# Performance work log

Measured on AMD Instinct MI355X. Metric: run time of the kernel, lower is better.

## Reference

```python
import jax, jax.numpy as jnp
import numpy as np

VOCAB_SIZE = 4096
D_EMBED = 256
BETA = 0.25  # unused: module returns raw commit_loss; beta applied by caller


def setup_inputs() -> dict:
    key = jax.random.key(0)
    k_h, k_e = jax.random.split(key)
    h = jax.random.normal(k_h, (16, D_EMBED, 32, 32), dtype=jnp.float32)
    embedding = jax.random.normal(k_e, (VOCAB_SIZE, D_EMBED), dtype=jnp.float32)
    return {"h": h, "embedding": embedding}


def reference(h, embedding):
    B, C, H, W = h.shape
    h = h.astype(jnp.float32)
    # (B, C, H, W) -> (N, C) with N = B*H*W
    h_flat = jnp.transpose(h, (0, 2, 3, 1)).reshape(-1, C)
    dist = (
        jnp.sum(h_flat * h_flat, axis=1, keepdims=True)
        + jnp.sum(embedding * embedding, axis=1)
        - 2.0 * jnp.einsum("nc,vc->nv", h_flat, embedding)
    )
    indices_flat = jnp.argmin(dist, axis=1)
    indices = indices_flat.reshape(B, H, W)
    # gather codebook vectors and restore (B, C, H, W)
    z_q = jnp.transpose(embedding[indices_flat].reshape(B, H, W, C), (0, 3, 1, 2))
    commit_loss = jnp.mean((h - jax.lax.stop_gradient(z_q)) ** 2)
    # straight-through estimator
    z_q_st = h + jax.lax.stop_gradient(z_q - h)
    return z_q_st, indices, commit_loss
```

## Files before the change

kernel.cpp:

```cpp
#include <hip/hip_runtime.h>

#define D 256
#define VOCAB 4096
#define NTOT 16384
#define N_OUT0 4194304

typedef _Float16 half8 __attribute__((ext_vector_type(8)));
typedef float f32x4 __attribute__((ext_vector_type(4)));

__device__ __forceinline__ void gld16(const void* g, void* l) {
    __builtin_amdgcn_global_load_lds(
        (const __attribute__((address_space(1))) void*)g,
        (__attribute__((address_space(3))) void*)l, 16, 0, 0);
}

__device__ __forceinline__ unsigned long long pack_key(float d, int v) {
    unsigned u = __float_as_uint(d);
    u ^= ((unsigned)((int)u >> 31)) | 0x80000000u;
    return ((unsigned long long)u << 32) | (unsigned)v;
}

__global__ __launch_bounds__(64) void k_prep(const float* __restrict__ emb,
                                             float* __restrict__ esq,
                                             unsigned long long* __restrict__ gbest,
                                             float* __restrict__ out2) {
    const int v = blockIdx.x, lane = threadIdx.x;
    float4 e = *(const float4*)(emb + (size_t)v * D + lane * 4);
    float s = e.x * e.x + e.y * e.y + e.z * e.z + e.w * e.w;
#pragma unroll
    for (int m = 32; m >= 1; m >>= 1) s += __shfl_xor(s, m, 64);
    if (lane == 0) esq[v] = s;
    if (v < NTOT / 64) gbest[(size_t)v * 64 + lane] = ~0ULL;
    if (v == 0 && lane == 0) out2[0] = 0.0f;
}

__global__ __launch_bounds__(256) void k_pack(const float* __restrict__ h,
                                              const float* __restrict__ emb,
                                              _Float16* __restrict__ Apk,
                                              _Float16* __restrict__ Bpk) {
    __shared__ float S[8192];
    const int tid = threadIdx.x;
    const int bid = blockIdx.x;
    if (bid < 512) {
        const int bm = bid >> 3, w = bid & 7;
        const int b = bm >> 2, p0 = (bm & 3) * 256;
        const float* src = h + ((size_t)b << 18) + p0;
#pragma unroll 4
        for (int cl = 0; cl < 32; ++cl)
            S[cl * 256 + tid] = src[(size_t)(w * 32 + cl) << 10 | (unsigned)tid];
        __syncthreads();
        _Float16* dstT = Apk + (size_t)bm * 131072 + (size_t)w * 16384;
#pragma unroll
        for (int i = 0; i < 4; ++i) {
            alignas(16) _Float16 hi[8], lo[8];
#pragma unroll
            for (int j = 0; j < 8; ++j) {
                float vv = S[(i * 8 + j) * 256 + tid];
                _Float16 hv = (_Float16)vv;
                hi[j] = hv;
                lo[j] = (_Float16)(vv - (float)hv);
            }
            _Float16* dst = dstT + i * 2048 + tid * 8;
            *(half8*)dst = *(half8*)hi;
            *(half8*)(dst + 8192) = *(half8*)lo;
        }
    } else {
        const int bid2 = bid - 512;
        const int bn = bid2 >> 3, w = bid2 & 7;
        const int v0 = bn * 128;
#pragma unroll 4
        for (int i = 0; i < 16; ++i) {
            int flat = i * 256 + tid;
            int r = flat >> 5, cl = flat & 31;
            S[cl * 129 + r] = emb[(size_t)(v0 + r) * D + w * 32 + cl];
        }
        __syncthreads();
        _Float16* dstT = Bpk + (size_t)bn * 65536 + (size_t)w * 8192;
#pragma unroll
        for (int i = 0; i < 2; ++i) {
            int s = i * 256 + tid;
            int q = s >> 7, r = s & 127;
            alignas(16) _Float16 hi[8], lo[8];
#pragma unroll
            for (int j = 0; j < 8; ++j) {
                float vv = S[(q * 8 + j) * 129 + r];
                _Float16 hv = (_Float16)vv;
                hi[j] = hv;
                lo[j] = (_Float16)(vv - (float)hv);
            }
            _Float16* dst = dstT + q * 1024 + r * 8;
            *(half8*)dst = *(half8*)hi;
            *(half8*)(dst + 4096) = *(half8*)lo;
        }
    }
}


#define STAGE_A_HI(W, NB) do { const _Float16* s_ = Ag + (W) * 16384; \
    gld16(s_ + tid * 8, As + (NB) + tid * 8); \
    gld16(s_ + 4096 + tid * 8, As + (NB) + 4096 + tid * 8); } while (0)
#define STAGE_A_LO(W, NB) do { const _Float16* s_ = Ag + (W) * 16384 + 8192; \
    gld16(s_ + tid * 8, As + (NB) + 8192 + tid * 8); \
    gld16(s_ + 4096 + tid * 8, As + (NB) + 12288 + tid * 8); } while (0)
#define STAGE_B_LO(W, NB) do { \
    gld16(Bg0 + (W) * 8192 + 4096 + tid * 8, Bs + (NB) + 4096 + tid * 8); \
    gld16(Bg1 + (W) * 8192 + 4096 + tid * 8, Bs + (NB) + 12288 + tid * 8); } while (0)
#define STAGE_B_HI(W, NB) do { \
    gld16(Bg0 + (W) * 8192 + tid * 8, Bs + (NB) + tid * 8); \
    gld16(Bg1 + (W) * 8192 + tid * 8, Bs + (NB) + 8192 + tid * 8); } while (0)

#define LOAD_AF(OFF) do { _Pragma("unroll") \
    for (int mt_ = 0; mt_ < 8; ++mt_) af[mt_] = *(const half8*)(aB + (OFF) + mt_ * 128); } while (0)
#define LOAD_BF(OFF) do { _Pragma("unroll") \
    for (int nt_ = 0; nt_ < 4; ++nt_) bf[nt_] = *(const half8*)(bB + (OFF) + nt_ * 128); } while (0)

#define MFMA32() do { \
    __builtin_amdgcn_s_setprio(1); \
    _Pragma("unroll") \
    for (int mt_ = 0; mt_ < 8; ++mt_) { \
      _Pragma("unroll") \
      for (int nt_ = 0; nt_ < 4; ++nt_) \
        acc[mt_][nt_] = __builtin_amdgcn_mfma_f32_16x16x32_f16(af[mt_], bf[nt_], acc[mt_][nt_], 0, 0, 0); \
    } \
    __builtin_amdgcn_s_setprio(0); \
  } while (0)

#define PHASE_END(N) do { \
    __builtin_amdgcn_sched_barrier(0); \
    asm volatile("s_waitcnt vmcnt(" #N ")" ::: "memory"); \
    __builtin_amdgcn_s_barrier(); } while (0)

__global__ __launch_bounds__(512, 2) void k_gemm(const _Float16* __restrict__ Apk,
                                                 const _Float16* __restrict__ Bpk,
                                                 const float* __restrict__ esq,
                                                 unsigned long long* __restrict__ gbest) {
    __shared__ alignas(16) _Float16 As[32768];
    __shared__ alignas(16) _Float16 Bs[32768];

    const int tid = threadIdx.x;
    const int bid = blockIdx.x;
    const int swz = (bid & 7) * 128 + (bid >> 3);
    const int bm = swz >> 4, bn = swz & 15;
    const int m0 = bm * 256, n0 = bn * 256;

    const _Float16* Ag = Apk + (size_t)bm * 131072;
    const _Float16* Bg0 = Bpk + (size_t)(2 * bn) * 65536;
    const _Float16* Bg1 = Bpk + (size_t)(2 * bn + 1) * 65536;

    STAGE_A_HI(0, 0);
    STAGE_B_LO(0, 0);
    STAGE_B_HI(0, 0);
    STAGE_A_LO(0, 0);

    const int wv = tid >> 6, l = tid & 63;
    const int wm = wv & 1, wn = wv >> 1;
    const int quad = l >> 4, j16 = l & 15;
    const int arow = wm * 128 + j16;
    const int brow = (wn & 1) * 64 + j16;
    const int bsub = wn >> 1;

    f32x4 acc[8][4];
#pragma unroll
    for (int i = 0; i < 8; ++i)
#pragma unroll
        for (int j = 0; j < 4; ++j) acc[i][j] = (f32x4)0.0f;

    asm volatile("s_waitcnt vmcnt(4)" ::: "memory");
    __builtin_amdgcn_s_barrier();

#pragma unroll 1
    for (int w = 0; w < 7; ++w) {
        const int cb = (w & 1) << 14, nb = cb ^ 16384;
        const _Float16* aB = As + cb + quad * 2048 + arow * 8;
        const _Float16* bB = Bs + cb + bsub * 8192 + quad * 1024 + brow * 8;
        half8 af[8], bf[4];

        LOAD_AF(0);
        LOAD_BF(4096);
        STAGE_A_HI(w + 1, nb);
        STAGE_B_LO(w + 1, nb);
        __builtin_amdgcn_s_barrier();
        MFMA32();
        PHASE_END(6);

        LOAD_BF(0);
        STAGE_B_HI(w + 1, nb);
        __builtin_amdgcn_s_barrier();
        MFMA32();
        PHASE_END(6);

        LOAD_AF(8192);
        STAGE_A_LO(w + 1, nb);
        __builtin_amdgcn_s_barrier();
        MFMA32();
        PHASE_END(4);
    }
    {
        const _Float16* aB = As + 16384 + quad * 2048 + arow * 8;
        const _Float16* bB = Bs + 16384 + bsub * 8192 + quad * 1024 + brow * 8;
        half8 af[8], bf[4];
        LOAD_AF(0);
        LOAD_BF(4096);
        __builtin_amdgcn_s_barrier();
        MFMA32();
        PHASE_END(2);
        LOAD_BF(0);
        __builtin_amdgcn_s_barrier();
        MFMA32();
        PHASE_END(0);
        LOAD_AF(8192);
        __builtin_amdgcn_s_barrier();
        MFMA32();
    }

    unsigned long long* red = (unsigned long long*)As;
    __syncthreads();
    if (tid < 256) red[tid] = ~0ULL;
    __syncthreads();

    float es[4];
#pragma unroll
    for (int nt = 0; nt < 4; ++nt) es[nt] = esq[n0 + wn * 64 + nt * 16 + j16];
#pragma unroll
    for (int mt = 0; mt < 8; ++mt) {
#pragma unroll
        for (int r = 0; r < 4; ++r) {
            unsigned long long best = ~0ULL;
#pragma unroll
            for (int nt = 0; nt < 4; ++nt) {
                float dv = es[nt] - 2.0f * acc[mt][nt][r];
                unsigned long long key = pack_key(dv, n0 + wn * 64 + nt * 16 + j16);
                best = key < best ? key : best;
            }
#pragma unroll
            for (int m = 8; m >= 1; m >>= 1) {
                unsigned long long o = __shfl_xor(best, m, 64);
                best = o < best ? o : best;
            }
            if (j16 == 0) atomicMin(&red[wm * 128 + mt * 16 + quad * 4 + r], best);
        }
    }
    __syncthreads();
    if (tid < 256) atomicMin(&gbest[m0 + tid], red[tid]);
}

__global__ __launch_bounds__(256) void k_gather(const float* __restrict__ h,
                                                const float* __restrict__ emb,
                                                const unsigned long long* __restrict__ gbest,
                                                float* __restrict__ out0,
                                                float* __restrict__ out1,
                                                float* __restrict__ out2) {
    __shared__ float zq[32][260];
    __shared__ float wred[4];
    const int tid = threadIdx.x;
    const int lane = tid & 63;
    const int w = tid >> 6;
    const int n0 = blockIdx.x * 32;
    const int b = n0 >> 10;
    const int p0 = n0 & 1023;
#pragma unroll
    for (int rr = 0; rr < 8; ++rr) {
        int r = w * 8 + rr;
        unsigned idx = (unsigned)(gbest[n0 + r] & 0xFFFFFFFFULL);
        float4 e4 = *(const float4*)(emb + (size_t)idx * D + lane * 4);
        *(float4*)&zq[r][lane * 4] = e4;
    }
    if (tid < 32) {
        unsigned idx = (unsigned)(gbest[n0 + tid] & 0xFFFFFFFFULL);
        out1[n0 + tid] = (float)idx;
    }
    __syncthreads();
    float lsum = 0.0f;
    const size_t base = ((size_t)b * D) << 10;
#pragma unroll 4
    for (int it = 0; it < 32; ++it) {
        int c = it * 8 + (tid >> 5);
        int pp = tid & 31;
        float z = zq[pp][c];
        size_t g = base + ((size_t)c << 10) + p0 + pp;
        float hv = h[g];
        out0[g] = hv + (z - hv);
        float d = hv - z;
        lsum = fmaf(d, d, lsum);
    }
#pragma unroll
    for (int m = 32; m >= 1; m >>= 1) lsum += __shfl_xor(lsum, m, 64);
    if (lane == 0) wred[w] = lsum;
    __syncthreads();
    if (tid == 0)
        atomicAdd(out2, (wred[0] + wred[1] + wred[2] + wred[3]) * (1.0f / (float)N_OUT0));
}

extern "C" void kernel_launch(void* const* d_in, const int* in_sizes, int n_in,
                              void* d_out, int out_size, void* d_ws, size_t ws_size,
                              hipStream_t stream) {
    const float* h = (const float*)d_in[0];
    const float* emb = (const float*)d_in[1];
    float* out0 = (float*)d_out;
    float* out1 = out0 + N_OUT0;
    float* out2 = out1 + NTOT;

    _Float16* Apk = (_Float16*)d_ws;
    _Float16* Bpk = (_Float16*)((char*)d_ws + 16777216);
    float* esq = (float*)((char*)d_ws + 16777216 + 4194304);
    unsigned long long* gbest = (unsigned long long*)((char*)d_ws + 16777216 + 4194304 + 16384);

    hipLaunchKernelGGL(k_prep, dim3(VOCAB), dim3(64), 0, stream, emb, esq, gbest, out2);
    hipLaunchKernelGGL(k_pack, dim3(768), dim3(256), 0, stream, h, emb, Apk, Bpk);
    hipLaunchKernelGGL(k_gemm, dim3(1024), dim3(512), 0, stream, Apk, Bpk, esq, gbest);
    hipLaunchKernelGGL(k_gather, dim3(NTOT / 32), dim3(256), 0, stream, h, emb, gbest, out0, out1, out2);
}
```

Before: 199.2 us.

## Fold codebook-norm prep into pack kernel and simplify GEMM double-buffer staging

Drops the separate k_prep launch and computes the codebook squared norms, the best-index reset and the loss zeroing in 64 extra blocks of k_pack. This removes one kernel launch and its dependency gap. The GEMM main loop replaces the three-phase staging, with its hand-tuned vmcnt waits and split barriers, with one bulk prefetch of the next whole K-slice into the other buffer, followed by a full __syncthreads per iteration. The simpler schedule may hide memory latency less finely, because every wave now waits for all outstanding loads at each iteration boundary.

```diff
diff --git a/kernel.cpp b/kernel.cpp
--- a/kernel.cpp
+++ b/kernel.cpp
@@ -20,24 +20,13 @@
     return ((unsigned long long)u << 32) | (unsigned)v;
 }
 
-__global__ __launch_bounds__(64) void k_prep(const float* __restrict__ emb,
-                                             float* __restrict__ esq,
-                                             unsigned long long* __restrict__ gbest,
-                                             float* __restrict__ out2) {
-    const int v = blockIdx.x, lane = threadIdx.x;
-    float4 e = *(const float4*)(emb + (size_t)v * D + lane * 4);
-    float s = e.x * e.x + e.y * e.y + e.z * e.z + e.w * e.w;
-#pragma unroll
-    for (int m = 32; m >= 1; m >>= 1) s += __shfl_xor(s, m, 64);
-    if (lane == 0) esq[v] = s;
-    if (v < NTOT / 64) gbest[(size_t)v * 64 + lane] = ~0ULL;
-    if (v == 0 && lane == 0) out2[0] = 0.0f;
-}
-
 __global__ __launch_bounds__(256) void k_pack(const float* __restrict__ h,
                                               const float* __restrict__ emb,
                                               _Float16* __restrict__ Apk,
-                                              _Float16* __restrict__ Bpk) {
+                                              _Float16* __restrict__ Bpk,
+                                              float* __restrict__ esq,
+                                              unsigned long long* __restrict__ gbest,
+                                              float* __restrict__ out2) {
     __shared__ float S[8192];
     const int tid = threadIdx.x;
     const int bid = blockIdx.x;
@@ -64,7 +53,7 @@
             *(half8*)dst = *(half8*)hi;
             *(half8*)(dst + 8192) = *(half8*)lo;
         }
-    } else {
+    } else if (bid < 768) {
         const int bid2 = bid - 512;
         const int bn = bid2 >> 3, w = bid2 & 7;
         const int v0 = bn * 128;
@@ -92,22 +81,37 @@
             *(half8*)dst = *(half8*)hi;
             *(half8*)(dst + 4096) = *(half8*)lo;
         }
-    }
-}
-
-
-#define STAGE_A_HI(W, NB) do { const _Float16* s_ = Ag + (W) * 16384; \
-    gld16(s_ + tid * 8, As + (NB) + tid * 8); \
-    gld16(s_ + 4096 + tid * 8, As + (NB) + 4096 + tid * 8); } while (0)
-#define STAGE_A_LO(W, NB) do { const _Float16* s_ = Ag + (W) * 16384 + 8192; \
-    gld16(s_ + tid * 8, As + (NB) + 8192 + tid * 8); \
-    gld16(s_ + 4096 + tid * 8, As + (NB) + 12288 + tid * 8); } while (0)
-#define STAGE_B_LO(W, NB) do { \
-    gld16(Bg0 + (W) * 8192 + 4096 + tid * 8, Bs + (NB) + 4096 + tid * 8); \
-    gld16(Bg1 + (W) * 8192 + 4096 + tid * 8, Bs + (NB) + 12288 + tid * 8); } while (0)
-#define STAGE_B_HI(W, NB) do { \
-    gld16(Bg0 + (W) * 8192 + tid * 8, Bs + (NB) + tid * 8); \
-    gld16(Bg1 + (W) * 8192 + tid * 8, Bs + (NB) + 8192 + tid * 8); } while (0)
+    } else {
+        const int pid = bid - 768;
+        const int lane = tid & 63, wv = tid >> 6;
+#pragma unroll 4
+        for (int i = 0; i < 16; ++i) {
+            int v = pid * 64 + i * 4 + wv;
+            float4 e = *(const float4*)(emb + (size_t)v * D + lane * 4);
+            float s = e.x * e.x + e.y * e.y + e.z * e.z + e.w * e.w;
+#pragma unroll
+            for (int m = 32; m >= 1; m >>= 1) s += __shfl_xor(s, m, 64);
+            if (lane == 0) esq[v] = s;
+        }
+        gbest[pid * 256 + tid] = ~0ULL;
+        if (pid == 0 && tid == 0) out2[0] = 0.0f;
+    }
+}
+
+
+#define STAGE_ALL(W, NB) do { \
+    const _Float16* sa_ = Ag + (W) * 16384; \
+    const _Float16* sb0_ = Bg0 + (W) * 8192; \
+    const _Float16* sb1_ = Bg1 + (W) * 8192; \
+    gld16(sa_ + tid * 8, As + (NB) + tid * 8); \
+    gld16(sa_ + 4096 + tid * 8, As + (NB) + 4096 + tid * 8); \
+    gld16(sa_ + 8192 + tid * 8, As + (NB) + 8192 + tid * 8); \
+    gld16(sa_ + 12288 + tid * 8, As + (NB) + 12288 + tid * 8); \
+    gld16(sb0_ + tid * 8, Bs + (NB) + tid * 8); \
+    gld16(sb0_ + 4096 + tid * 8, Bs + (NB) + 4096 + tid * 8); \
+    gld16(sb1_ + tid * 8, Bs + (NB) + 8192 + tid * 8); \
+    gld16(sb1_ + 4096 + tid * 8, Bs + (NB) + 12288 + tid * 8); \
+} while (0)
 
 #define LOAD_AF(OFF) do { _Pragma("unroll") \
     for (int mt_ = 0; mt_ < 8; ++mt_) af[mt_] = *(const half8*)(aB + (OFF) + mt_ * 128); } while (0)
@@ -125,11 +129,6 @@
     __builtin_amdgcn_s_setprio(0); \
   } while (0)
 
-#define PHASE_END(N) do { \
-    __builtin_amdgcn_sched_barrier(0); \
-    asm volatile("s_waitcnt vmcnt(" #N ")" ::: "memory"); \
-    __builtin_amdgcn_s_barrier(); } while (0)
-
 __global__ __launch_bounds__(512, 2) void k_gemm(const _Float16* __restrict__ Apk,
                                                  const _Float16* __restrict__ Bpk,
                                                  const float* __restrict__ esq,
@@ -147,10 +146,7 @@
     const _Float16* Bg0 = Bpk + (size_t)(2 * bn) * 65536;
     const _Float16* Bg1 = Bpk + (size_t)(2 * bn + 1) * 65536;
 
-    STAGE_A_HI(0, 0);
-    STAGE_B_LO(0, 0);
-    STAGE_B_HI(0, 0);
-    STAGE_A_LO(0, 0);
+    STAGE_ALL(0, 0);
 
     const int wv = tid >> 6, l = tid & 63;
     const int wm = wv & 1, wn = wv >> 1;
@@ -165,56 +161,26 @@
 #pragma unroll
         for (int j = 0; j < 4; ++j) acc[i][j] = (f32x4)0.0f;
 
-    asm volatile("s_waitcnt vmcnt(4)" ::: "memory");
-    __builtin_amdgcn_s_barrier();
+    __syncthreads();
 
 #pragma unroll 1
-    for (int w = 0; w < 7; ++w) {
+    for (int w = 0; w < 8; ++w) {
         const int cb = (w & 1) << 14, nb = cb ^ 16384;
         const _Float16* aB = As + cb + quad * 2048 + arow * 8;
         const _Float16* bB = Bs + cb + bsub * 8192 + quad * 1024 + brow * 8;
-        half8 af[8], bf[4];
-
-        LOAD_AF(0);
-        LOAD_BF(4096);
-        STAGE_A_HI(w + 1, nb);
-        STAGE_B_LO(w + 1, nb);
-        __builtin_amdgcn_s_barrier();
-        MFMA32();
-        PHASE_END(6);
-
-        LOAD_BF(0);
-        STAGE_B_HI(w + 1, nb);
-        __builtin_amdgcn_s_barrier();
-        MFMA32();
-        PHASE_END(6);
-
-        LOAD_AF(8192);
-        STAGE_A_LO(w + 1, nb);
-        __builtin_amdgcn_s_barrier();
-        MFMA32();
-        PHASE_END(4);
-    }
-    {
-        const _Float16* aB = As + 16384 + quad * 2048 + arow * 8;
-        const _Float16* bB = Bs + 16384 + bsub * 8192 + quad * 1024 + brow * 8;
+        if (w < 7) STAGE_ALL(w + 1, nb);
         half8 af[8], bf[4];
         LOAD_AF(0);
         LOAD_BF(4096);
-        __builtin_amdgcn_s_barrier();
         MFMA32();
-        PHASE_END(2);
         LOAD_BF(0);
-        __builtin_amdgcn_s_barrier();
         MFMA32();
-        PHASE_END(0);
         LOAD_AF(8192);
-        __builtin_amdgcn_s_barrier();
         MFMA32();
+        __syncthreads();
     }
 
     unsigned long long* red = (unsigned long long*)As;
-    __syncthreads();
     if (tid < 256) red[tid] = ~0ULL;
     __syncthreads();
 
@@ -305,8 +271,7 @@
     float* esq = (float*)((char*)d_ws + 16777216 + 4194304);
     unsigned long long* gbest = (unsigned long long*)((char*)d_ws + 16777216 + 4194304 + 16384);
 
-    hipLaunchKernelGGL(k_prep, dim3(VOCAB), dim3(64), 0, stream, emb, esq, gbest, out2);
-    hipLaunchKernelGGL(k_pack, dim3(768), dim3(256), 0, stream, h, emb, Apk, Bpk);
+    hipLaunchKernelGGL(k_pack, dim3(832), dim3(256), 0, stream, h, emb, Apk, Bpk, esq, gbest, out2);
     hipLaunchKernelGGL(k_gemm, dim3(1024), dim3(512), 0, stream, Apk, Bpk, esq, gbest);
     hipLaunchKernelGGL(k_gather, dim3(NTOT / 32), dim3(256), 0, stream, h, emb, gbest, out0, out1, out2);
 }
```

Measured after the change: 201.1 us. About the same (+1.0%).
